# Kernel tuning notes

Hardware: AMD Instinct MI355X
Metric: run time of the kernel (lower is better)

## Reference

```python
import jax, jax.numpy as jnp
import numpy as np
import math

B, S, D, H, V = 2, 2048, 512, 4, 32000
WINDOWS = [None, 128, 512, None]  # per-head attention windows (None = unlimited)


def setup_inputs() -> dict:
    key = jax.random.key(0)
    ks = jax.random.split(key, 8)
    input_ids = jax.random.randint(ks[0], (B, S), 0, V, dtype=jnp.int64)
    padding_mask = jnp.zeros((B, S), dtype=bool)  # True = pad
    embed_table = jax.random.normal(ks[1], (V, D), dtype=jnp.float32) * 0.02
    self_factors = jnp.full((H,), 0.1, dtype=jnp.float32)
    distance_alphas = jnp.full((H,), 0.1, dtype=jnp.float32)
    # torch Linear weights: [out_features, in_features], xavier-uniform init
    lim_f = math.sqrt(6.0 / (H * D + D))
    fusion_w = jax.random.uniform(ks[2], (D, H * D), jnp.float32, -lim_f, lim_f)
    fusion_b = jnp.zeros((D,), jnp.float32)
    lim_o = math.sqrt(6.0 / (D + V))
    out_w = jax.random.uniform(ks[3], (V, D), jnp.float32, -lim_o, lim_o)
    out_b = jnp.zeros((V,), jnp.float32)
    return {
        "input_ids": input_ids,
        "padding_mask": padding_mask,
        "embed_table": embed_table,
        "self_factors": self_factors,
        "distance_alphas": distance_alphas,
        "fusion_w": fusion_w,
        "fusion_b": fusion_b,
        "out_w": out_w,
        "out_b": out_b,
    }


def reference(input_ids, padding_mask, embed_table, self_factors,
              distance_alphas, fusion_w, fusion_b, out_w, out_b):
    b, s = input_ids.shape
    d = embed_table.shape[1]
    h = self_factors.shape[0]

    emb = embed_table[input_ids]  # [B,S,D]

    pos = jnp.arange(s)
    dist = jnp.abs(pos[:, None] - pos[None, :])          # [S,S]
    causal = pos[None, :] > pos[:, None]                  # [S,S] strict upper triangle
    eye = dist == 0                                       # [S,S]

    # shared raw scores, computed once (same for all heads)
    base = jnp.einsum('bqd,bkd->bqk', emb, emb) / math.sqrt(d)  # [B,S,S]

    # per-head distance decay bias: [H,S,S]
    decay = 1.0 / (1.0 + distance_alphas[:, None, None] * dist.astype(jnp.float32))

    scores = base[None, :, :, :] * decay[:, None, :, :]   # [H,B,S,S]
    # diagonal self-factor scaling
    scores = jnp.where(eye[None, None],
                       scores * self_factors[:, None, None, None], scores)

    # per-head window mask (None -> window >= S, never masks)
    win = jnp.array([s if w is None else w for w in WINDOWS[:h]])
    window_mask = dist[None, :, :] > win[:, None, None]   # [H,S,S]

    # key padding mask, diagonal exempted (as in original)
    key_pad = padding_mask[:, None, :] & (~eye[None])      # [B,S,S]

    full_mask = (window_mask[:, None] | causal[None, None] | key_pad[None])  # [H,B,S,S]
    scores = jnp.where(full_mask, -jnp.inf, scores)

    attn = jax.nn.softmax(scores, axis=-1)                 # [H,B,S,S]
    ctx = jnp.einsum('hbqk,bkd->hbqd', attn, emb)          # [H,B,S,D]

    concat = jnp.moveaxis(ctx, 0, 2).reshape(b, s, h * d)  # [B,S,H*D]
    fused = concat @ fusion_w.T + fusion_b                 # [B,S,D]
    logits = fused @ out_w.T + out_b                       # [B,S,V]
    return logits
```

## Files before the change

### kernel.cpp

```cpp
#include <hip/hip_runtime.h>
#include <hip/hip_bf16.h>
#include <stdint.h>

#define BB 2
#define SB 2048
#define DD 512
#define HH 4
#define VV 32000

typedef __attribute__((ext_vector_type(4))) float f32x4;
typedef __attribute__((ext_vector_type(8))) short bf16x8;
typedef __attribute__((ext_vector_type(4))) unsigned short us4;

__device__ __forceinline__ unsigned short f2bf(float f) {
    unsigned u = __float_as_uint(f);
    u += 0x7fffu + ((u >> 16) & 1u);
    return (unsigned short)(u >> 16);
}

__device__ __forceinline__ __attribute__((address_space(3))) unsigned int*
as_lds(void* p) {
    return (__attribute__((address_space(3))) unsigned int*)(unsigned)(uintptr_t)p;
}
__device__ __forceinline__ const __attribute__((address_space(1))) unsigned int*
as_gbl(const void* p) {
    return (const __attribute__((address_space(1))) unsigned int*)(uintptr_t)p;
}

__device__ __forceinline__ bf16x8 ldsrd64(const unsigned short* base, int row, int c) {
    return *(const bf16x8*)((const char*)base + row * 128 + ((c ^ (row & 7)) << 4));
}

__global__ void k_prep(const int* __restrict__ ids, const float* __restrict__ tbl,
                       const float* __restrict__ als,
                       const float* __restrict__ fw, const float* __restrict__ ow,
                       unsigned short* __restrict__ outw_bf, unsigned short* __restrict__ fusw_bf,
                       unsigned short* __restrict__ emb, unsigned short* __restrict__ embT,
                       float* __restrict__ dtab, float* __restrict__ lsum)
{
    __shared__ unsigned short TT[64][72];
    const int bid = blockIdx.x, t = threadIdx.x;

    if (bid < 2000) {
        int base = bid * 8192 + t * 4;
#pragma unroll
        for (int it = 0; it < 8; ++it) {
            int i = base + it * 1024;
            float4 v = *(const float4*)(ow + i);
            us4 o; o.x = f2bf(v.x); o.y = f2bf(v.y); o.z = f2bf(v.z); o.w = f2bf(v.w);
            *(us4*)(outw_bf + i) = o;
        }
    } else if (bid < 2256) {
        int base = (bid - 2000) * 4096 + t * 4;
#pragma unroll
        for (int it = 0; it < 4; ++it) {
            int i = base + it * 1024;
            float4 v = *(const float4*)(fw + i);
            us4 o; o.x = f2bf(v.x); o.y = f2bf(v.y); o.z = f2bf(v.z); o.w = f2bf(v.w);
            *(us4*)(fusw_bf + i) = o;
        }
    } else if (bid < 6352) {
        int row = bid - 2256;
        int id = ids[row];
        if (id < 0) id = 0;
        if (id >= VV) id = VV - 1;
        const float* s = tbl + (size_t)id * DD;
        unsigned short* d = emb + (size_t)row * DD;
        d[t]       = f2bf(s[t]);
        d[t + 256] = f2bf(s[t + 256]);
    } else if (bid < 6448) {
        int i = (bid - 6352) * 256 + t;
        if (i < HH * SB) {
            int h = i >> 11, dd = i & (SB - 1);
            dtab[i] = 0.04419417382415922f / (1.f + als[h] * (float)dd);
        } else {
            lsum[i - HH * SB] = 0.f;
        }
    } else {
        int bid2 = bid - 6448;
        const int d0 = (bid2 & 7) * 64, s0 = ((bid2 >> 3) & 31) * 64, b = bid2 >> 8;
        {
            int s = t >> 2, c16 = (t & 3) * 16;
            int id = ids[b * SB + s0 + s];
            if (id < 0) id = 0;
            if (id >= VV) id = VV - 1;
            const float* src = tbl + (size_t)id * DD + d0 + c16;
#pragma unroll
            for (int q4 = 0; q4 < 4; ++q4) {
                float4 v = *(const float4*)(src + q4 * 4);
                TT[c16 + q4 * 4 + 0][s] = f2bf(v.x);
                TT[c16 + q4 * 4 + 1][s] = f2bf(v.y);
                TT[c16 + q4 * 4 + 2][s] = f2bf(v.z);
                TT[c16 + q4 * 4 + 3][s] = f2bf(v.w);
            }
        }
        __syncthreads();
        {
            int d = t >> 2, sc = (t & 3) * 16;
            bf16x8 o0, o1;
#pragma unroll
            for (int j = 0; j < 8; ++j) {
                o0[j] = (short)TT[d][sc + j];
                o1[j] = (short)TT[d][sc + 8 + j];
            }
            unsigned short* dst = embT + ((size_t)(b * DD + d0 + d)) * SB + s0 + sc;
            *(bf16x8*)dst = o0;
            *(bf16x8*)(dst + 8) = o1;
        }
    }
}

__launch_bounds__(256, 2)
__global__ void k_base(const unsigned short* __restrict__ emb,
                       const unsigned char* __restrict__ pad,
                       const float* __restrict__ sfs,
                       const float* __restrict__ dtab,
                       unsigned short* __restrict__ P,
                       float* __restrict__ lsum)
{
    const int kt = blockIdx.x, qt = blockIdx.y, b = blockIdx.z;
    if (kt > qt + 1) return;
    const int tid = threadIdx.x, lane = tid & 63, wv = tid >> 6;
    const int l15 = lane & 15, g = lane >> 4;

    if (kt == qt + 1) {
        int row = tid >> 2, cb = (tid & 3) * 16;
        int4 z = {0, 0, 0, 0};
#pragma unroll
        for (int h = 0; h < 4; ++h) {
            unsigned short* Ph = P + (((size_t)(h * 2 + b)) * SB + qt * 64 + row) * SB + kt * 64 + cb;
            *(int4*)Ph = z;
            *(int4*)(Ph + 8) = z;
        }
        return;
    }

    __shared__ __align__(16) unsigned short Ql[64 * 128];
    __shared__ __align__(16) unsigned short Kl[64 * 128];

    const int q = qt * 64 + wv * 16 + l15;

    f32x4 zero4 = {0.f, 0.f, 0.f, 0.f};
    f32x4 cc[4];
#pragma unroll
    for (int c = 0; c < 4; ++c) cc[c] = zero4;

    for (int dc = 0; dc < 4; ++dc) {
        const int d0 = dc * 128;
        __syncthreads();
#pragma unroll
        for (int i = 0; i < 4; ++i) {
            int flat = (i * 256 + tid) * 8;
            int row = flat >> 7;
            int ch  = (flat >> 3) & 15;
            int scol = ((ch ^ (row & 15)) << 3);
            __builtin_amdgcn_global_load_lds(
                as_gbl(emb + ((size_t)(b * SB + qt * 64 + row)) * DD + d0 + scol),
                as_lds(Ql + flat), 16, 0, 0);
            __builtin_amdgcn_global_load_lds(
                as_gbl(emb + ((size_t)(b * SB + kt * 64 + row)) * DD + d0 + scol),
                as_lds(Kl + flat), 16, 0, 0);
        }
        asm volatile("s_waitcnt vmcnt(0)" ::: "memory");
        __syncthreads();

#pragma unroll
        for (int dsl = 0; dsl < 4; ++dsl) {
            int chr = (dsl * 4 + g);
            bf16x8 qf = *(const bf16x8*)(Ql + (wv * 16 + l15) * 128 + ((chr ^ l15) << 3));
#pragma unroll
            for (int c = 0; c < 4; ++c) {
                bf16x8 kf = *(const bf16x8*)(Kl + (c * 16 + l15) * 128 + ((chr ^ l15) << 3));
                cc[c] = __builtin_amdgcn_mfma_f32_16x16x32_bf16(kf, qf, cc[c], 0, 0, 0);
            }
        }
    }

    unsigned long long padm = __ballot(pad[(size_t)b * SB + kt * 64 + lane] != 0);

    const int wins[4] = {1 << 30, 128, 512, 1 << 30};
#pragma unroll
    for (int h = 0; h < 4; ++h) {
        const int win = wins[h];
        if (kt * 64 + win + 192 < qt * 64) continue;
        const float sf = sfs[h];
        const float* dth = dtab + h * SB;
        float rsum = 0.f;
        unsigned short pb[4][4];
#pragma unroll
        for (int c = 0; c < 4; ++c) {
#pragma unroll
            for (int r = 0; r < 4; ++r) {
                int kk = kt * 64 + c * 16 + 4 * g + r;
                int dist = q - kk;
                float p = 0.f;
                if (dist >= 0 && dist <= win &&
                    ((dist == 0) || !((padm >> (c * 16 + 4 * g + r)) & 1ull))) {
                    float s = cc[c][r] * dth[dist];
                    if (dist == 0) s *= sf;
                    p = __expf(s);
                }
                rsum += p;
                pb[c][r] = f2bf(p);
            }
        }
        unsigned short* Ph = P + (((size_t)(h * 2 + b)) * SB + q) * SB + kt * 64;
#pragma unroll
        for (int c = 0; c < 4; ++c) {
            us4 o;
            o.x = pb[c][0]; o.y = pb[c][1]; o.z = pb[c][2]; o.w = pb[c][3];
            *(us4*)(Ph + c * 16 + 4 * g) = o;
        }
        rsum += __shfl_xor(rsum, 16, 64);
        rsum += __shfl_xor(rsum, 32, 64);
        if (lane < 16)
            atomicAdd(&lsum[((size_t)(h * 2 + b)) * SB + q], rsum);
    }
}

__launch_bounds__(256, 2)
__global__ void k_pv(const unsigned short* __restrict__ P,
                     const unsigned short* __restrict__ embT,
                     const float* __restrict__ lsum,
                     unsigned short* __restrict__ concat)
{
    const int t64 = blockIdx.x, b = blockIdx.y, h = blockIdx.z;
    const int mt = t64 >> 2, nt = t64 & 3;
    const int Q0 = mt * 128;
    const int win = (h == 1) ? 128 : (h == 2) ? 512 : (1 << 30);
    int klo = Q0 - win - 64; if (klo < 0) klo = 0; klo &= ~63;
    const int khi = Q0 + 128;

    __shared__ __align__(16) unsigned short Al[128 * 32];
    __shared__ __align__(16) unsigned short Bl[128 * 32];

    const int tid = threadIdx.x, lane = tid & 63, wv = tid >> 6;
    const int wm = (wv >> 1) * 64, wn = (wv & 1) * 64;
    const int l15 = lane & 15, g = lane >> 4;

    f32x4 zero4 = {0.f, 0.f, 0.f, 0.f};
    f32x4 acc[4][4];
#pragma unroll
    for (int i = 0; i < 4; ++i)
#pragma unroll
        for (int j = 0; j < 4; ++j) acc[i][j] = zero4;

    const unsigned short* Ab = P + (((size_t)(h * 2 + b)) * SB + Q0) * SB;
    const unsigned short* Bb = embT + ((size_t)(b * DD + nt * 128)) * SB;

    for (int k0 = klo; k0 < khi; k0 += 32) {
        __syncthreads();
#pragma unroll
        for (int s = 0; s < 2; ++s) {
            int e = (s * 256 + tid) * 8;
            int row = e >> 5, col = e & 31;
            __builtin_amdgcn_global_load_lds(as_gbl(Ab + (size_t)row * SB + k0 + col),
                                             as_lds(Al + e), 16, 0, 0);
            __builtin_amdgcn_global_load_lds(as_gbl(Bb + (size_t)row * SB + k0 + col),
                                             as_lds(Bl + e), 16, 0, 0);
        }
        asm volatile("s_waitcnt vmcnt(0)" ::: "memory");
        __syncthreads();

        bf16x8 af[4], bfr[4];
#pragma unroll
        for (int i = 0; i < 4; ++i) {
            af[i]  = *(const bf16x8*)(Al + (wm + i * 16 + l15) * 32 + 8 * g);
            bfr[i] = *(const bf16x8*)(Bl + (wn + i * 16 + l15) * 32 + 8 * g);
        }
#pragma unroll
        for (int i = 0; i < 4; ++i)
#pragma unroll
            for (int j = 0; j < 4; ++j)
                acc[i][j] = __builtin_amdgcn_mfma_f32_16x16x32_bf16(af[i], bfr[j], acc[i][j], 0, 0, 0);
    }

    const float* ls = lsum + ((size_t)(h * 2 + b)) * SB;
    unsigned short* cb = concat + ((size_t)(b * SB)) * (HH * DD) + h * DD + nt * 128;
#pragma unroll
    for (int i = 0; i < 4; ++i) {
        int rowb = wm + i * 16 + g * 4;
        float inv[4];
#pragma unroll
        for (int rr = 0; rr < 4; ++rr) inv[rr] = 1.f / ls[Q0 + rowb + rr];
#pragma unroll
        for (int j = 0; j < 4; ++j) {
            int col = wn + j * 16 + l15;
#pragma unroll
            for (int rr = 0; rr < 4; ++rr)
                cb[(size_t)(Q0 + rowb + rr) * (HH * DD) + col] = f2bf(acc[i][j][rr] * inv[rr]);
        }
    }
}

template <int OUTF32>
__launch_bounds__(256, 2)
__global__ void k_gemm_bt(const unsigned short* __restrict__ A,
                          const unsigned short* __restrict__ Bt,
                          const float* __restrict__ bias,
                          void* __restrict__ Cout,
                          int M, int N, int K)
{
    const int nMt = M >> 7;
    const int nwg = gridDim.x;
    int bid = blockIdx.x;
    int q = nwg >> 3, r = nwg & 7;
    int x = bid & 7, o = bid >> 3;
    int wg = (x < r ? x * (q + 1) : r * (q + 1) + (x - r) * q) + o;
    const int mt = wg % nMt, nt = wg / nMt;

    __shared__ __align__(16) unsigned short Al[128 * 32];
    __shared__ __align__(16) unsigned short Bl[128 * 32];

    const int tid = threadIdx.x;
    const int lane = tid & 63;
    const int wv = tid >> 6;
    const int wm = (wv >> 1) * 64, wn = (wv & 1) * 64;
    const int l15 = lane & 15, g = lane >> 4;

    f32x4 zero4 = {0.f, 0.f, 0.f, 0.f};
    f32x4 acc[4][4];
#pragma unroll
    for (int i = 0; i < 4; ++i)
#pragma unroll
        for (int j = 0; j < 4; ++j) acc[i][j] = zero4;

    const unsigned short* Ab = A + (size_t)mt * 128 * K;
    const unsigned short* Bb = Bt + (size_t)nt * 128 * K;

    for (int k0 = 0; k0 < K; k0 += 32) {
        __syncthreads();
#pragma unroll
        for (int s = 0; s < 2; ++s) {
            int e = (s * 256 + tid) * 8;
            int row = e >> 5, col = e & 31;
            __builtin_amdgcn_global_load_lds(as_gbl(Ab + (size_t)row * K + k0 + col),
                                             as_lds(Al + e), 16, 0, 0);
            __builtin_amdgcn_global_load_lds(as_gbl(Bb + (size_t)row * K + k0 + col),
                                             as_lds(Bl + e), 16, 0, 0);
        }
        asm volatile("s_waitcnt vmcnt(0)" ::: "memory");
        __syncthreads();

        bf16x8 af[4], bfr[4];
#pragma unroll
        for (int i = 0; i < 4; ++i) {
            af[i]  = *(const bf16x8*)(Al + (wm + i * 16 + l15) * 32 + 8 * g);
            bfr[i] = *(const bf16x8*)(Bl + (wn + i * 16 + l15) * 32 + 8 * g);
        }
#pragma unroll
        for (int i = 0; i < 4; ++i)
#pragma unroll
            for (int j = 0; j < 4; ++j)
                acc[i][j] = __builtin_amdgcn_mfma_f32_16x16x32_bf16(af[i], bfr[j], acc[i][j], 0, 0, 0);
    }

#pragma unroll
    for (int i = 0; i < 4; ++i) {
        int rowb = mt * 128 + wm + i * 16 + g * 4;
#pragma unroll
        for (int j = 0; j < 4; ++j) {
            int col = nt * 128 + wn + j * 16 + l15;
            float bv = bias[col];
            if (OUTF32) {
                float* C = (float*)Cout;
#pragma unroll
                for (int rr = 0; rr < 4; ++rr)
                    C[(size_t)(rowb + rr) * N + col] = acc[i][j][rr] + bv;
            } else {
                unsigned short* C = (unsigned short*)Cout;
#pragma unroll
                for (int rr = 0; rr < 4; ++rr)
                    C[(size_t)(rowb + rr) * N + col] = f2bf(acc[i][j][rr] + bv);
            }
        }
    }
}

__launch_bounds__(512, 1)
__global__ void k_logits(const unsigned short* __restrict__ A,
                         const unsigned short* __restrict__ Bt,
                         const float* __restrict__ bias,
                         float* __restrict__ Cout,
                         int M, int N, int K)
{
    const int nMt = M >> 8;
    const int nwg = gridDim.x;
    int bid = blockIdx.x;
    int q = nwg >> 3, r = nwg & 7;
    int x = bid & 7, o = bid >> 3;
    int wg = (x < r ? x * (q + 1) : r * (q + 1) + (x - r) * q) + o;
    const int mt = wg % nMt, nt = wg / nMt;

    __shared__ __align__(16) char smem[131072];

    const int tid = threadIdx.x, lane = tid & 63, wv = tid >> 6;
    const int wr = wv >> 2, wc = wv & 3;
    const int l15 = lane & 15, g = lane >> 4;

    f32x4 zero4 = {0.f, 0.f, 0.f, 0.f};
    f32x4 acc[8][4];
#pragma unroll
    for (int i = 0; i < 8; ++i)
#pragma unroll
        for (int j = 0; j < 4; ++j) acc[i][j] = zero4;

    const unsigned short* Ab = A + (size_t)mt * 256 * K;
    const unsigned short* Bb = Bt + (size_t)nt * 256 * K;

    const unsigned short* As[4];
    const unsigned short* Bs[4];
    int ldstA[4], ldstB[4];
#pragma unroll
    for (int j = 0; j < 4; ++j) {
        int ch = tid + j * 512;
        int row = ch >> 3, cpos = ch & 7;
        int scol = ((cpos ^ (row & 7)) << 3);
        As[j] = Ab + (size_t)row * K + scol;
        Bs[j] = Bb + (size_t)row * K + scol;
        ldstA[j] = ch * 16;
        ldstB[j] = 65536 + ch * 16;
    }

#define STG(bufi_, k0_) {                                                              \
    _Pragma("unroll")                                                                  \
    for (int j = 0; j < 4; ++j)                                                        \
        __builtin_amdgcn_global_load_lds(as_gbl(As[j] + (k0_)),                        \
            as_lds(smem + (bufi_) * 32768 + ldstA[j]), 16, 0, 0);                      \
    _Pragma("unroll")                                                                  \
    for (int j = 0; j < 4; ++j)                                                        \
        __builtin_amdgcn_global_load_lds(as_gbl(Bs[j] + (k0_)),                        \
            as_lds(smem + (bufi_) * 32768 + ldstB[j]), 16, 0, 0); }

    STG(0, 0);
    __syncthreads();

    for (int t = 0; t < 8; ++t) {
        const int cur = t & 1;
        if (t < 7) STG(cur ^ 1, (t + 1) * 64);
        const unsigned short* Ar = (const unsigned short*)(smem + cur * 32768);
        const unsigned short* Br = (const unsigned short*)(smem + cur * 32768 + 65536);
#pragma unroll
        for (int s = 0; s < 2; ++s) {
            bf16x8 bf[4], af[8];
#pragma unroll
            for (int n = 0; n < 4; ++n)
                bf[n] = ldsrd64(Br, wc * 64 + n * 16 + l15, s * 4 + g);
#pragma unroll
            for (int m = 0; m < 8; ++m)
                af[m] = ldsrd64(Ar, wr * 128 + m * 16 + l15, s * 4 + g);
            __builtin_amdgcn_s_setprio(1);
#pragma unroll
            for (int m = 0; m < 8; ++m)
#pragma unroll
                for (int n = 0; n < 4; ++n)
                    acc[m][n] = __builtin_amdgcn_mfma_f32_16x16x32_bf16(af[m], bf[n], acc[m][n], 0, 0, 0);
            __builtin_amdgcn_s_setprio(0);
        }
        __syncthreads();
    }
#undef STG

    const int mrow = mt * 256;
    const int ncol = nt * 256;
    float* Cl = (float*)smem;
    float bvj[4];
#pragma unroll
    for (int j = 0; j < 4; ++j) bvj[j] = bias[ncol + wc * 64 + j * 16 + l15];
    const int srow = tid >> 4;
    const int scol = (tid & 15) * 4;
    const float* Crd = Cl + srow * 258 + scol;
#pragma unroll
    for (int mc = 0; mc < 8; ++mc) {
        if (wr == (mc >> 2)) {
            int ibase = (mc & 3) * 2;
#pragma unroll
            for (int ii = 0; ii < 2; ++ii) {
                int i = ibase + ii;
                int lr = ii * 16 + g * 4;
#pragma unroll
                for (int j = 0; j < 4; ++j)
#pragma unroll
                    for (int rr = 0; rr < 4; ++rr)
                        Cl[(lr + rr) * 258 + wc * 64 + j * 16 + l15] = acc[i][j][rr] + bvj[j];
            }
        }
        __syncthreads();
        {
            float* gp = Cout + (size_t)(mrow + mc * 32 + srow) * N + ncol + scol;
#pragma unroll
            for (int it = 0; it < 4; ++it)
                *(float4*)(gp + it * 64) = *(const float4*)(Crd + it * 64);
        }
        __syncthreads();
    }
}

extern "C" void kernel_launch(void* const* d_in, const int* in_sizes, int n_in,
                              void* d_out, int out_size, void* d_ws, size_t ws_size,
                              hipStream_t stream)
{
    const int*           ids = (const int*)d_in[0];
    const unsigned char* pad = (const unsigned char*)d_in[1];
    const float*         tbl = (const float*)d_in[2];
    const float*         sfs = (const float*)d_in[3];
    const float*         als = (const float*)d_in[4];
    const float*         fw  = (const float*)d_in[5];
    const float*         fb  = (const float*)d_in[6];
    const float*         ow  = (const float*)d_in[7];
    const float*         ob  = (const float*)d_in[8];
    float* logits = (float*)d_out;

    char* ws = (char*)d_ws;
    unsigned short* outw_bf = (unsigned short*)(ws);
    unsigned short* fusw_bf = (unsigned short*)(ws + 32768000);
    unsigned short* emb_bf  = (unsigned short*)(ws + 34865152);
    unsigned short* concat  = (unsigned short*)(ws + 39059456);
    unsigned short* fused   = (unsigned short*)(ws + 55836672);

    char* ob_scratch = (char*)d_out;
    unsigned short* P    = (unsigned short*)(ob_scratch);
    unsigned short* embT = (unsigned short*)(ob_scratch + 67108864);
    float*          dtab = (float*)(ob_scratch + 71303168);
    float*          lsum = (float*)(ob_scratch + 71335936);

    k_prep<<<6960, 256, 0, stream>>>(ids, tbl, als, fw, ow,
                                     outw_bf, fusw_bf, emb_bf, embT, dtab, lsum);

    dim3 bg(32, 32, BB);
    k_base<<<bg, 256, 0, stream>>>(emb_bf, pad, sfs, dtab, P, lsum);

    dim3 pg(64, BB, HH);
    k_pv<<<pg, 256, 0, stream>>>(P, embT, lsum, concat);

    k_gemm_bt<0><<<32 * 4, 256, 0, stream>>>(concat, fusw_bf, fb, fused, BB * SB, DD, HH * DD);
    k_logits<<<16 * 125, 512, 0, stream>>>(fused, outw_bf, ob, logits, BB * SB, VV, DD);
}
```

Baseline: 373.1 us.

## Shrink logits GEMM LDS footprint to allow two workgroups per CU

The logits GEMM drops from a double-buffered pipeline with K=64 stages to a single-buffered loop with K=32 stages. This cuts LDS from 128 KB to about 33 KB, with the swizzle adapted to 64-byte rows, and raises launch bounds so two workgroups can share a CU. The aim is to hide latency with more resident waves rather than with in-kernel prefetch. In exchange, each iteration waits for all its loads (vmcnt(0)) and runs two barriers, so global-load latency is no longer overlapped within a workgroup.

```diff
diff --git a/kernel.cpp b/kernel.cpp
--- a/kernel.cpp
+++ b/kernel.cpp
@@ -27,8 +27,8 @@
     return (const __attribute__((address_space(1))) unsigned int*)(uintptr_t)p;
 }
 
-__device__ __forceinline__ bf16x8 ldsrd64(const unsigned short* base, int row, int c) {
-    return *(const bf16x8*)((const char*)base + row * 128 + ((c ^ (row & 7)) << 4));
+__device__ __forceinline__ bf16x8 ldsrd32(const unsigned short* base, int row, int c) {
+    return *(const bf16x8*)((const char*)base + row * 64 + (((c) ^ (row & 3)) << 4));
 }
 
 __global__ void k_prep(const int* __restrict__ ids, const float* __restrict__ tbl,
@@ -377,7 +377,7 @@
     }
 }
 
-__launch_bounds__(512, 1)
+__launch_bounds__(512, 2)
 __global__ void k_logits(const unsigned short* __restrict__ A,
                          const unsigned short* __restrict__ Bt,
                          const float* __restrict__ bias,
@@ -392,7 +392,7 @@
     int wg = (x < r ? x * (q + 1) : r * (q + 1) + (x - r) * q) + o;
     const int mt = wg % nMt, nt = wg / nMt;
 
-    __shared__ __align__(16) char smem[131072];
+    __shared__ __align__(16) char smem[33024];
 
     const int tid = threadIdx.x, lane = tid & 63, wv = tid >> 6;
     const int wr = wv >> 2, wc = wv & 3;
@@ -408,59 +408,49 @@
     const unsigned short* Ab = A + (size_t)mt * 256 * K;
     const unsigned short* Bb = Bt + (size_t)nt * 256 * K;
 
-    const unsigned short* As[4];
-    const unsigned short* Bs[4];
-    int ldstA[4], ldstB[4];
-#pragma unroll
-    for (int j = 0; j < 4; ++j) {
+    const unsigned short* As[2];
+    const unsigned short* Bs[2];
+    int ldstA[2], ldstB[2];
+#pragma unroll
+    for (int j = 0; j < 2; ++j) {
         int ch = tid + j * 512;
-        int row = ch >> 3, cpos = ch & 7;
-        int scol = ((cpos ^ (row & 7)) << 3);
+        int row = ch >> 2, cpos = ch & 3;
+        int scol = ((cpos ^ (row & 3)) << 3);
         As[j] = Ab + (size_t)row * K + scol;
         Bs[j] = Bb + (size_t)row * K + scol;
         ldstA[j] = ch * 16;
-        ldstB[j] = 65536 + ch * 16;
-    }
-
-#define STG(bufi_, k0_) {                                                              \
-    _Pragma("unroll")                                                                  \
-    for (int j = 0; j < 4; ++j)                                                        \
-        __builtin_amdgcn_global_load_lds(as_gbl(As[j] + (k0_)),                        \
-            as_lds(smem + (bufi_) * 32768 + ldstA[j]), 16, 0, 0);                      \
-    _Pragma("unroll")                                                                  \
-    for (int j = 0; j < 4; ++j)                                                        \
-        __builtin_amdgcn_global_load_lds(as_gbl(Bs[j] + (k0_)),                        \
-            as_lds(smem + (bufi_) * 32768 + ldstB[j]), 16, 0, 0); }
-
-    STG(0, 0);
+        ldstB[j] = 16384 + ch * 16;
+    }
+
+    for (int k0 = 0; k0 < K; k0 += 32) {
+        __syncthreads();
+#pragma unroll
+        for (int j = 0; j < 2; ++j) {
+            __builtin_amdgcn_global_load_lds(as_gbl(As[j] + k0), as_lds(smem + ldstA[j]), 16, 0, 0);
+            __builtin_amdgcn_global_load_lds(as_gbl(Bs[j] + k0), as_lds(smem + ldstB[j]), 16, 0, 0);
+        }
+        asm volatile("s_waitcnt vmcnt(0)" ::: "memory");
+        __syncthreads();
+
+        const unsigned short* Ar = (const unsigned short*)smem;
+        const unsigned short* Br = (const unsigned short*)(smem + 16384);
+        bf16x8 bf[4], af[8];
+#pragma unroll
+        for (int n = 0; n < 4; ++n)
+            bf[n] = ldsrd32(Br, wc * 64 + n * 16 + l15, g);
+#pragma unroll
+        for (int m = 0; m < 8; ++m)
+            af[m] = ldsrd32(Ar, wr * 128 + m * 16 + l15, g);
+        __builtin_amdgcn_s_setprio(1);
+#pragma unroll
+        for (int m = 0; m < 8; ++m)
+#pragma unroll
+            for (int n = 0; n < 4; ++n)
+                acc[m][n] = __builtin_amdgcn_mfma_f32_16x16x32_bf16(af[m], bf[n], acc[m][n], 0, 0, 0);
+        __builtin_amdgcn_s_setprio(0);
+    }
+
     __syncthreads();
-
-    for (int t = 0; t < 8; ++t) {
-        const int cur = t & 1;
-        if (t < 7) STG(cur ^ 1, (t + 1) * 64);
-        const unsigned short* Ar = (const unsigned short*)(smem + cur * 32768);
-        const unsigned short* Br = (const unsigned short*)(smem + cur * 32768 + 65536);
-#pragma unroll
-        for (int s = 0; s < 2; ++s) {
-            bf16x8 bf[4], af[8];
-#pragma unroll
-            for (int n = 0; n < 4; ++n)
-                bf[n] = ldsrd64(Br, wc * 64 + n * 16 + l15, s * 4 + g);
-#pragma unroll
-            for (int m = 0; m < 8; ++m)
-                af[m] = ldsrd64(Ar, wr * 128 + m * 16 + l15, s * 4 + g);
-            __builtin_amdgcn_s_setprio(1);
-#pragma unroll
-            for (int m = 0; m < 8; ++m)
-#pragma unroll
-                for (int n = 0; n < 4; ++n)
-                    acc[m][n] = __builtin_amdgcn_mfma_f32_16x16x32_bf16(af[m], bf[n], acc[m][n], 0, 0, 0);
-            __builtin_amdgcn_s_setprio(0);
-        }
-        __syncthreads();
-    }
-#undef STG
-
     const int mrow = mt * 256;
     const int ncol = nt * 256;
     float* Cl = (float*)smem;
```

After: 450.2 us. +20.7%, slower.

## Double-buffer LDS staging in score, PV and GEMM kernels

Applied to the files above, without the earlier changes.

The score, PV and bias-GEMM kernels now use ping-pong LDS buffers. The next K/D slice is issued with global_load_lds while MFMAs run on the current slice, so global-load latency overlaps compute. The PV kernel also widens its K step from 32 to 64 and uses an XOR-swizzled LDS layout to reduce bank conflicts. In exchange, LDS use per block roughly doubles, which can lower occupancy. Correctness now depends on the barrier at the end of each iteration waiting for the outstanding async loads.

```diff
diff --git a/kernel.cpp b/kernel.cpp
--- a/kernel.cpp
+++ b/kernel.cpp
@@ -135,46 +135,49 @@
         return;
     }
 
-    __shared__ __align__(16) unsigned short Ql[64 * 128];
-    __shared__ __align__(16) unsigned short Kl[64 * 128];
+    __shared__ __align__(16) unsigned short Ql[2][64 * 128];
+    __shared__ __align__(16) unsigned short Kl[2][64 * 128];
 
     const int q = qt * 64 + wv * 16 + l15;
+
+#define STAGEB(buf_, dc_) {                                                            \
+    _Pragma("unroll")                                                                  \
+    for (int i = 0; i < 4; ++i) {                                                      \
+        int flat = (i * 256 + tid) * 8;                                                \
+        int row = flat >> 7;                                                           \
+        int ch  = (flat >> 3) & 15;                                                    \
+        int scol = ((ch ^ (row & 15)) << 3);                                           \
+        __builtin_amdgcn_global_load_lds(                                              \
+            as_gbl(emb + ((size_t)(b * SB + qt * 64 + row)) * DD + (dc_) * 128 + scol),\
+            as_lds(Ql[buf_] + flat), 16, 0, 0);                                        \
+        __builtin_amdgcn_global_load_lds(                                              \
+            as_gbl(emb + ((size_t)(b * SB + kt * 64 + row)) * DD + (dc_) * 128 + scol),\
+            as_lds(Kl[buf_] + flat), 16, 0, 0);                                        \
+    } }
 
     f32x4 zero4 = {0.f, 0.f, 0.f, 0.f};
     f32x4 cc[4];
 #pragma unroll
     for (int c = 0; c < 4; ++c) cc[c] = zero4;
 
+    STAGEB(0, 0);
+    __syncthreads();
     for (int dc = 0; dc < 4; ++dc) {
-        const int d0 = dc * 128;
-        __syncthreads();
-#pragma unroll
-        for (int i = 0; i < 4; ++i) {
-            int flat = (i * 256 + tid) * 8;
-            int row = flat >> 7;
-            int ch  = (flat >> 3) & 15;
-            int scol = ((ch ^ (row & 15)) << 3);
-            __builtin_amdgcn_global_load_lds(
-                as_gbl(emb + ((size_t)(b * SB + qt * 64 + row)) * DD + d0 + scol),
-                as_lds(Ql + flat), 16, 0, 0);
-            __builtin_amdgcn_global_load_lds(
-                as_gbl(emb + ((size_t)(b * SB + kt * 64 + row)) * DD + d0 + scol),
-                as_lds(Kl + flat), 16, 0, 0);
-        }
-        asm volatile("s_waitcnt vmcnt(0)" ::: "memory");
-        __syncthreads();
-
+        const int cur = dc & 1;
+        if (dc < 3) STAGEB(cur ^ 1, dc + 1);
 #pragma unroll
         for (int dsl = 0; dsl < 4; ++dsl) {
             int chr = (dsl * 4 + g);
-            bf16x8 qf = *(const bf16x8*)(Ql + (wv * 16 + l15) * 128 + ((chr ^ l15) << 3));
+            bf16x8 qf = *(const bf16x8*)(Ql[cur] + (wv * 16 + l15) * 128 + ((chr ^ l15) << 3));
 #pragma unroll
             for (int c = 0; c < 4; ++c) {
-                bf16x8 kf = *(const bf16x8*)(Kl + (c * 16 + l15) * 128 + ((chr ^ l15) << 3));
+                bf16x8 kf = *(const bf16x8*)(Kl[cur] + (c * 16 + l15) * 128 + ((chr ^ l15) << 3));
                 cc[c] = __builtin_amdgcn_mfma_f32_16x16x32_bf16(kf, qf, cc[c], 0, 0, 0);
             }
         }
-    }
+        __syncthreads();
+    }
+#undef STAGEB
 
     unsigned long long padm = __ballot(pad[(size_t)b * SB + kt * 64 + lane] != 0);
 
@@ -230,9 +233,10 @@
     const int win = (h == 1) ? 128 : (h == 2) ? 512 : (1 << 30);
     int klo = Q0 - win - 64; if (klo < 0) klo = 0; klo &= ~63;
     const int khi = Q0 + 128;
-
-    __shared__ __align__(16) unsigned short Al[128 * 32];
-    __shared__ __align__(16) unsigned short Bl[128 * 32];
+    const int nsteps = (khi - klo) >> 6;
+
+    __shared__ __align__(16) unsigned short Pl[2][128 * 64];
+    __shared__ __align__(16) unsigned short Vl[2][128 * 64];
 
     const int tid = threadIdx.x, lane = tid & 63, wv = tid >> 6;
     const int wm = (wv >> 1) * 64, wn = (wv & 1) * 64;
@@ -248,32 +252,50 @@
     const unsigned short* Ab = P + (((size_t)(h * 2 + b)) * SB + Q0) * SB;
     const unsigned short* Bb = embT + ((size_t)(b * DD + nt * 128)) * SB;
 
-    for (int k0 = klo; k0 < khi; k0 += 32) {
-        __syncthreads();
+    const unsigned short* Ps[4];
+    const unsigned short* Vs[4];
+    int ldst[4];
+#pragma unroll
+    for (int j = 0; j < 4; ++j) {
+        int ch = j * 256 + tid;
+        int row = ch >> 3, cpos = ch & 7;
+        int scol = ((cpos ^ (row & 7)) << 3);
+        Ps[j] = Ab + (size_t)row * SB + scol;
+        Vs[j] = Bb + (size_t)row * SB + scol;
+        ldst[j] = ch * 16;
+    }
+
+#define STAGEPV(buf_, k0_) {                                                           \
+    _Pragma("unroll")                                                                  \
+    for (int j = 0; j < 4; ++j) {                                                      \
+        __builtin_amdgcn_global_load_lds(as_gbl(Ps[j] + (k0_)),                        \
+            as_lds((char*)Pl[buf_] + ldst[j]), 16, 0, 0);                              \
+        __builtin_amdgcn_global_load_lds(as_gbl(Vs[j] + (k0_)),                        \
+            as_lds((char*)Vl[buf_] + ldst[j]), 16, 0, 0);                              \
+    } }
+
+    STAGEPV(0, klo);
+    __syncthreads();
+    for (int t = 0; t < nsteps; ++t) {
+        const int cur = t & 1;
+        if (t + 1 < nsteps) STAGEPV(cur ^ 1, klo + (t + 1) * 64);
 #pragma unroll
         for (int s = 0; s < 2; ++s) {
-            int e = (s * 256 + tid) * 8;
-            int row = e >> 5, col = e & 31;
-            __builtin_amdgcn_global_load_lds(as_gbl(Ab + (size_t)row * SB + k0 + col),
-                                             as_lds(Al + e), 16, 0, 0);
-            __builtin_amdgcn_global_load_lds(as_gbl(Bb + (size_t)row * SB + k0 + col),
-                                             as_lds(Bl + e), 16, 0, 0);
-        }
-        asm volatile("s_waitcnt vmcnt(0)" ::: "memory");
-        __syncthreads();
-
-        bf16x8 af[4], bfr[4];
-#pragma unroll
-        for (int i = 0; i < 4; ++i) {
-            af[i]  = *(const bf16x8*)(Al + (wm + i * 16 + l15) * 32 + 8 * g);
-            bfr[i] = *(const bf16x8*)(Bl + (wn + i * 16 + l15) * 32 + 8 * g);
-        }
-#pragma unroll
-        for (int i = 0; i < 4; ++i)
-#pragma unroll
-            for (int j = 0; j < 4; ++j)
-                acc[i][j] = __builtin_amdgcn_mfma_f32_16x16x32_bf16(af[i], bfr[j], acc[i][j], 0, 0, 0);
-    }
+            bf16x8 af[4], bfr[4];
+#pragma unroll
+            for (int i = 0; i < 4; ++i) {
+                af[i]  = ldsrd64(Pl[cur], wm + i * 16 + l15, s * 4 + g);
+                bfr[i] = ldsrd64(Vl[cur], wn + i * 16 + l15, s * 4 + g);
+            }
+#pragma unroll
+            for (int i = 0; i < 4; ++i)
+#pragma unroll
+                for (int j = 0; j < 4; ++j)
+                    acc[i][j] = __builtin_amdgcn_mfma_f32_16x16x32_bf16(af[i], bfr[j], acc[i][j], 0, 0, 0);
+        }
+        __syncthreads();
+    }
+#undef STAGEPV
 
     const float* ls = lsum + ((size_t)(h * 2 + b)) * SB;
     unsigned short* cb = concat + ((size_t)(b * SB)) * (HH * DD) + h * DD + nt * 128;
@@ -309,8 +331,8 @@
     int wg = (x < r ? x * (q + 1) : r * (q + 1) + (x - r) * q) + o;
     const int mt = wg % nMt, nt = wg / nMt;
 
-    __shared__ __align__(16) unsigned short Al[128 * 32];
-    __shared__ __align__(16) unsigned short Bl[128 * 32];
+    __shared__ __align__(16) unsigned short Al[2][128 * 32];
+    __shared__ __align__(16) unsigned short Bl[2][128 * 32];
 
     const int tid = threadIdx.x;
     const int lane = tid & 63;
@@ -328,32 +350,37 @@
     const unsigned short* Ab = A + (size_t)mt * 128 * K;
     const unsigned short* Bb = Bt + (size_t)nt * 128 * K;
 
-    for (int k0 = 0; k0 < K; k0 += 32) {
-        __syncthreads();
-#pragma unroll
-        for (int s = 0; s < 2; ++s) {
-            int e = (s * 256 + tid) * 8;
-            int row = e >> 5, col = e & 31;
-            __builtin_amdgcn_global_load_lds(as_gbl(Ab + (size_t)row * K + k0 + col),
-                                             as_lds(Al + e), 16, 0, 0);
-            __builtin_amdgcn_global_load_lds(as_gbl(Bb + (size_t)row * K + k0 + col),
-                                             as_lds(Bl + e), 16, 0, 0);
-        }
-        asm volatile("s_waitcnt vmcnt(0)" ::: "memory");
-        __syncthreads();
-
+#define STAGEF(buf_, k0_) {                                                            \
+    _Pragma("unroll")                                                                  \
+    for (int s = 0; s < 2; ++s) {                                                      \
+        int e = (s * 256 + tid) * 8;                                                   \
+        int row = e >> 5, col = e & 31;                                                \
+        __builtin_amdgcn_global_load_lds(as_gbl(Ab + (size_t)row * K + (k0_) + col),   \
+                                         as_lds(Al[buf_] + e), 16, 0, 0);              \
+        __builtin_amdgcn_global_load_lds(as_gbl(Bb + (size_t)row * K + (k0_) + col),   \
+                                         as_lds(Bl[buf_] + e), 16, 0, 0);              \
+    } }
+
+    const int nk = K >> 5;
+    STAGEF(0, 0);
+    __syncthreads();
+    for (int t = 0; t < nk; ++t) {
+        const int cur = t & 1;
+        if (t + 1 < nk) STAGEF(cur ^ 1, (t + 1) * 32);
         bf16x8 af[4], bfr[4];
 #pragma unroll
         for (int i = 0; i < 4; ++i) {
-            af[i]  = *(const bf16x8*)(Al + (wm + i * 16 + l15) * 32 + 8 * g);
-            bfr[i] = *(const bf16x8*)(Bl + (wn + i * 16 + l15) * 32 + 8 * g);
+            af[i]  = *(const bf16x8*)(Al[cur] + (wm + i * 16 + l15) * 32 + 8 * g);
+            bfr[i] = *(const bf16x8*)(Bl[cur] + (wn + i * 16 + l15) * 32 + 8 * g);
         }
 #pragma unroll
         for (int i = 0; i < 4; ++i)
 #pragma unroll
             for (int j = 0; j < 4; ++j)
                 acc[i][j] = __builtin_amdgcn_mfma_f32_16x16x32_bf16(af[i], bfr[j], acc[i][j], 0, 0, 0);
-    }
+        __syncthreads();
+    }
+#undef STAGEF
 
 #pragma unroll
     for (int i = 0; i < 4; ++i) {
```

After: 367.6 us. Within noise of the previous version (-1.5%).
